# Kernel optimization log

Measured on AMD Instinct MI355X. Metric: run time of the kernel, lower is better.

The kernel has to match this reference:

```python
import jax, jax.numpy as jnp
import numpy as np
from jax import lax

K = 3
STRIDE = 1
PAD = 1


def setup_inputs() -> dict:
    key = jax.random.key(0)
    k0, k1, k2, k3 = jax.random.split(key, 4)
    B, C, H, W, O = 8, 128, 64, 64, 128
    x = jax.random.normal(k0, (B, C, H, W), jnp.float32)
    # offset_conv: Conv2d(C, 2*K*K) - small init so sampled offsets stay moderate
    w_off = jax.random.normal(k1, (2 * K * K, C, K, K), jnp.float32) * 0.01
    b_off = jnp.zeros((2 * K * K,), jnp.float32)
    # deform_conv main weight, kaiming-ish scale
    w_def = jax.random.normal(k2, (O, C, K, K), jnp.float32) * (1.0 / np.sqrt(C * K * K))
    b_def = jax.random.normal(k3, (O,), jnp.float32) * 0.01
    return {"x": x, "w_off": w_off, "b_off": b_off, "w_def": w_def, "b_def": b_def}


def _conv2d(x, w, b, stride, pad):
    y = lax.conv_general_dilated(
        x, w, window_strides=(stride, stride), padding=[(pad, pad), (pad, pad)],
        dimension_numbers=("NCHW", "OIHW", "NCHW"))
    return y + b[None, :, None, None]


def _bilinear_sample(x, py, px):
    """x: [B,C,Hin,Win]; py,px: [B,KK,H,W] -> [B,C,KK,H,W] with zero padding."""
    B, C, Hin, Win = x.shape
    iy0f = jnp.floor(py)
    ix0f = jnp.floor(px)
    wy = py - iy0f  # grad of floor is 0, so d(wy)/d(py) = 1 (matches deform conv)
    wx = px - ix0f
    iy0 = iy0f.astype(jnp.int32)
    ix0 = ix0f.astype(jnp.int32)

    def gather(iy, ix):
        valid = (iy >= 0) & (iy < Hin) & (ix >= 0) & (ix < Win)
        iyc = jnp.clip(iy, 0, Hin - 1)
        ixc = jnp.clip(ix, 0, Win - 1)
        g = jax.vmap(lambda xb, a, b: xb[:, a, b])(x, iyc, ixc)  # [B,C,KK,H,W]
        return g * valid[:, None].astype(x.dtype)

    v00 = gather(iy0, ix0)
    v01 = gather(iy0, ix0 + 1)
    v10 = gather(iy0 + 1, ix0)
    v11 = gather(iy0 + 1, ix0 + 1)
    wy_ = wy[:, None]
    wx_ = wx[:, None]
    return (v00 * (1 - wy_) * (1 - wx_) + v01 * (1 - wy_) * wx_
            + v10 * wy_ * (1 - wx_) + v11 * wy_ * wx_)


def reference(x, w_off, b_off, w_def, b_def):
    B, C, H, W = x.shape
    O = w_def.shape[0]
    KK = K * K
    # 1) standard conv predicting offsets: [B, 2*KK, Hout, Wout]
    offsets = _conv2d(x, w_off, b_off, STRIDE, PAD)
    Hout, Wout = offsets.shape[2], offsets.shape[3]
    # torchvision layout: interleaved (dy, dx) per kernel tap
    off = offsets.reshape(B, KK, 2, Hout, Wout)
    off_y, off_x = off[:, :, 0], off[:, :, 1]  # [B,KK,Hout,Wout]
    # 2) base sampling grid per kernel tap
    kys, kxs = jnp.meshgrid(jnp.arange(K), jnp.arange(K), indexing="ij")
    kys = kys.reshape(KK).astype(jnp.float32)
    kxs = kxs.reshape(KK).astype(jnp.float32)
    hs = (jnp.arange(Hout) * STRIDE - PAD).astype(jnp.float32)
    ws = (jnp.arange(Wout) * STRIDE - PAD).astype(jnp.float32)
    base_y = hs[None, :, None] + kys[:, None, None]  # [KK,Hout,1]
    base_x = ws[None, None, :] + kxs[:, None, None]  # [KK,1,Wout]
    py = base_y[None] + off_y  # [B,KK,Hout,Wout]
    px = base_x[None] + off_x
    # 3) gather bilinear-sampled patches then dense contraction (im2col GEMM)
    sampled = _bilinear_sample(x, py, px)  # [B,C,KK,Hout,Wout]
    out = jnp.einsum("bckhw,ock->bohw", sampled, w_def.reshape(O, C, KK))
    return out + b_def[None, :, None, None]
```

## Files before the change

### kernel.cpp

```cpp
#include <hip/hip_runtime.h>
#include <hip/hip_bf16.h>

#define BB 8
#define CC 128
#define HH 64
#define WW 64
#define OO 128
#define NJ 18
#define HW 4096

typedef unsigned short u16;
typedef unsigned int u32;
typedef __attribute__((ext_vector_type(8))) __bf16 bf16x8;
typedef __attribute__((ext_vector_type(4))) float f32x4;

__device__ __forceinline__ u16 f2bf(float f) {
    u32 u = __float_as_uint(f);
    u += 0x7fffu + ((u >> 16) & 1u);
    return (u16)(u >> 16);
}
__device__ __forceinline__ float bflo(u32 u) { return __uint_as_float(u << 16); }
__device__ __forceinline__ float bfhi(u32 u) { return __uint_as_float(u & 0xffff0000u); }
__device__ __forceinline__ u32 pk2bf(float s0, float s1) {
    union { __hip_bfloat162 h; u32 u; } cv;
    cv.h = __float22bfloat162_rn(make_float2(s0, s1));
    return cv.u;
}

__global__ __launch_bounds__(256)
void k_xT(const float* __restrict__ x, u16* __restrict__ xT) {
    __shared__ float tile[64][129];
    const int t = threadIdx.x;
    const int b = blockIdx.x >> 6;
    const int hw0 = (blockIdx.x & 63) << 6;
    const float* xb = x + (size_t)b * CC * HW + hw0;
    const int tw = t & 63, tc = t >> 6;
#pragma unroll
    for (int r = 0; r < 32; ++r) {
        int c = r * 4 + tc;
        tile[tw][c] = xb[c * HW + tw];
    }
    __syncthreads();
    u16* dst = xT + ((size_t)b * HW + hw0) * CC;
#pragma unroll
    for (int r = 0; r < 4; ++r) {
        int item = t + (r << 8);
        int seg = item & 15, hw = item >> 4;
        union { u32 d[4]; uint4 v; } p;
#pragma unroll
        for (int i = 0; i < 4; ++i)
            p.d[i] = pk2bf(tile[hw][seg * 8 + 2 * i], tile[hw][seg * 8 + 2 * i + 1]);
        *(uint4*)&dst[hw * CC + seg * 8] = p.v;
    }
}

__global__ void k_prep(const float* __restrict__ w_def,
                       const float* __restrict__ w_off,
                       u16* __restrict__ wT, u16* __restrict__ wA) {
    int idx = blockIdx.x * 256 + threadIdx.x;
    if (idx < 9 * OO * CC) {
        int c = idx & 127, o = (idx >> 7) & 127, kk = idx >> 14;
        wT[idx] = f2bf(w_def[(o * CC + c) * 9 + kk]);
    }
    if (idx < 32 * 1152) {
        int k = idx % 1152, j = idx / 1152;
        int q = k >> 7, c = k & 127;
        wA[idx] = (j < NJ) ? f2bf(w_off[(j * CC + c) * 9 + q]) : (u16)0;
    }
}

__global__ __launch_bounds__(256, 2)
void k_off(const u16* __restrict__ xT, const u16* __restrict__ wA,
           const float* __restrict__ b_off, float* __restrict__ offs) {
    __shared__ u16 s_x[198 * 128];
    const int t = threadIdx.x, lane = t & 63, wv = t >> 6;
    const int posl = lane & 15, kg = lane >> 4;
    const int b = blockIdx.x & 7, h = blockIdx.x >> 3;

    for (int it = t; it < 3168; it += 256) {
        int seg = it & 15, pix = it >> 4;
        int r = pix / 66, wp = pix - r * 66;
        int y = h - 1 + r, w = wp - 1;
        uint4 v = make_uint4(0, 0, 0, 0);
        if (y >= 0 && y < HH && w >= 0 && w < WW)
            v = *(const uint4*)&xT[((size_t)(b * HW) + y * WW + w) * CC + seg * 8];
        *(uint4*)&s_x[pix * 128 + ((seg ^ (pix & 15)) * 8)] = v;
    }
    __syncthreads();

    f32x4 acc0 = {0.f, 0.f, 0.f, 0.f}, acc1 = {0.f, 0.f, 0.f, 0.f};
    for (int q = 0; q < 9; ++q) {
        int qy = q / 3, qx = q - qy * 3;
        int pix = qy * 66 + (wv * 16 + posl) + qx;
        int prow = pix * 128, pxor = pix & 15;
#pragma unroll
        for (int ki = 0; ki < 4; ++ki) {
            int ks = q * 4 + ki;
            int cidx = ki * 4 + kg;
            bf16x8 bfr = *(const bf16x8*)&s_x[prow + ((cidx ^ pxor) * 8)];
            bf16x8 a0 = *(const bf16x8*)&wA[posl * 1152 + ks * 32 + kg * 8];
            bf16x8 a1 = *(const bf16x8*)&wA[(16 + posl) * 1152 + ks * 32 + kg * 8];
            acc0 = __builtin_amdgcn_mfma_f32_16x16x32_bf16(a0, bfr, acc0, 0, 0, 0);
            acc1 = __builtin_amdgcn_mfma_f32_16x16x32_bf16(a1, bfr, acc1, 0, 0, 0);
        }
    }
    const int pos = wv * 16 + posl;
#pragma unroll
    for (int r = 0; r < 4; ++r) {
        int j = kg * 4 + r;
        offs[(b * NJ + j) * HW + h * WW + pos] = acc0[r] + b_off[j];
    }
#pragma unroll
    for (int r = 0; r < 4; ++r) {
        int j = 16 + kg * 4 + r;
        if (j < NJ) offs[(b * NJ + j) * HW + h * WW + pos] = acc1[r] + b_off[j];
    }
}

__global__ __launch_bounds__(256, 3)
void k_main(const u16* __restrict__ xT, const float* __restrict__ offs,
            const u16* __restrict__ wT, const float* __restrict__ b_def,
            float* __restrict__ out) {
    __shared__ u16 s_wt[128 * 128];
    __shared__ u16 s_samp[16 * 520];

    const int t = threadIdx.x, lane = t & 63, wv = t >> 6;
    const int posl = lane & 15, rg = lane >> 4;
    const int b = blockIdx.x & 7;
    const int h = blockIdx.x >> 3;
    const int w = lane;
    const char* xb = (const char*)xT + (size_t)b * (HW * CC * 2);

    f32x4 acc[8];
#pragma unroll
    for (int mt = 0; mt < 8; ++mt) acc[mt] = (f32x4){0.f, 0.f, 0.f, 0.f};

    for (int kk = 0; kk < 9; ++kk) {
#pragma unroll
        for (int r = 0; r < 8; ++r) {
            int item = r * 256 + t;
            int o = item >> 4, sg = item & 15;
            *(uint4*)&s_wt[o * 128 + ((sg ^ (o & 15)) * 8)] =
                *(const uint4*)&wT[kk * (OO * CC) + item * 8];
        }
        int ky = kk / 3, kx = kk - ky * 3;
        float oy = offs[(b * NJ + 2 * kk) * HW + h * WW + w];
        float ox = offs[(b * NJ + 2 * kk + 1) * HW + h * WW + w];
        float py = (float)(h - 1 + ky) + oy;
        float px = (float)(w - 1 + kx) + ox;
        float fy = floorf(py), fx = floorf(px);
        int iy0 = (int)fy, ix0 = (int)fx;
        float wy = py - fy, wx = px - fx;
        int iy1 = iy0 + 1, ix1 = ix0 + 1;
        float my0 = (iy0 >= 0 && iy0 < HH) ? 1.0f : 0.0f;
        float my1 = (iy1 >= 0 && iy1 < HH) ? 1.0f : 0.0f;
        float mx0 = (ix0 >= 0 && ix0 < WW) ? 1.0f : 0.0f;
        float mx1 = (ix1 >= 0 && ix1 < WW) ? 1.0f : 0.0f;
        int iy0c = min(max(iy0, 0), HH - 1), iy1c = min(max(iy1, 0), HH - 1);
        int ix0c = min(max(ix0, 0), WW - 1), ix1c = min(max(ix1, 0), WW - 1);
        float wy1 = 1.0f - wy, wx1 = 1.0f - wx;
        float cwx = my0 * mx0 * wy1 * wx1, cwy = my0 * mx1 * wy1 * wx;
        float cwz = my1 * mx0 * wy * wx1,  cww = my1 * mx1 * wy * wx;
        int cox = (iy0c * WW + ix0c) << 8, coy = (iy0c * WW + ix1c) << 8;
        int coz = (iy1c * WW + ix0c) << 8, cow = (iy1c * WW + ix1c) << 8;

#pragma unroll
        for (int j = 0; j < 4; ++j) {
            const int seg = 4 * wv + j;
            const char* base = xb + seg * 16;
            uint4 q00 = *(const uint4*)(base + cox);
            uint4 q01 = *(const uint4*)(base + coy);
            uint4 q10 = *(const uint4*)(base + coz);
            uint4 q11 = *(const uint4*)(base + cow);
            const u32* u00 = (const u32*)&q00;
            const u32* u01 = (const u32*)&q01;
            const u32* u10 = (const u32*)&q10;
            const u32* u11 = (const u32*)&q11;
            union { u32 d[4]; uint4 v; } p;
#pragma unroll
            for (int i = 0; i < 4; ++i) {
                float s0 = cwx * bflo(u00[i]) + cwy * bflo(u01[i])
                         + cwz * bflo(u10[i]) + cww * bflo(u11[i]);
                float s1 = cwx * bfhi(u00[i]) + cwy * bfhi(u01[i])
                         + cwz * bfhi(u10[i]) + cww * bfhi(u11[i]);
                p.d[i] = pk2bf(s0, s1);
            }
            *(uint4*)&s_samp[seg * 520 + lane * 8] = p.v;
        }
        __syncthreads();

#pragma unroll
        for (int ct = 0; ct < 4; ++ct) {
            const int cidx = ct * 4 + rg;
            bf16x8 bfr = *(const bf16x8*)&s_samp[cidx * 520 + (wv * 16 + posl) * 8];
#pragma unroll
            for (int mt = 0; mt < 8; ++mt) {
                bf16x8 af = *(const bf16x8*)&s_wt[(mt * 16 + posl) * 128 + ((cidx ^ posl) * 8)];
                acc[mt] = __builtin_amdgcn_mfma_f32_16x16x32_bf16(af, bfr, acc[mt], 0, 0, 0);
            }
        }
        __syncthreads();
    }

    const int wout = wv * 16 + posl;
#pragma unroll
    for (int mt = 0; mt < 8; ++mt) {
#pragma unroll
        for (int r = 0; r < 4; ++r) {
            int o = mt * 16 + rg * 4 + r;
            out[((b * OO + o) * HH + h) * WW + wout] = acc[mt][r] + b_def[o];
        }
    }
}

extern "C" void kernel_launch(void* const* d_in, const int* in_sizes, int n_in,
                              void* d_out, int out_size, void* d_ws, size_t ws_size,
                              hipStream_t stream) {
    const float* x     = (const float*)d_in[0];
    const float* w_off = (const float*)d_in[1];
    const float* b_off = (const float*)d_in[2];
    const float* w_def = (const float*)d_in[3];
    const float* b_def = (const float*)d_in[4];
    float* out = (float*)d_out;

    float* offs = (float*)d_ws;
    u16*   xT   = (u16*)(offs + BB * NJ * HW);
    u16*   wT   = xT + (size_t)BB * HW * CC;
    u16*   wA   = wT + 9 * OO * CC;

    k_xT  <<<512, 256, 0, stream>>>(x, xT);
    k_prep<<<576, 256, 0, stream>>>(w_def, w_off, wT, wA);
    k_off <<<512, 256, 0, stream>>>(xT, wA, b_off, offs);
    k_main<<<512, 256, 0, stream>>>(xT, offs, wT, b_def, out);
}
```

Measured before the change: 159.7 us.

## Load weight fragments directly to registers and swap MFMA operand roles in main kernel

Removes the per-tap staging of the 128x128 weight slice into shared memory; each wave now reads its 32-output-channel slice of weights straight from global memory into registers. Sampled patches become the A operand (positions along M) with an XOR-swizzled 64x128 layout, and the sampling work is redistributed so four threads share a position and each handles four channel segments. Outputs are written as float4 along width. This shrinks LDS use and the sync-heavy weight copy, at the cost of global (L2) weight reads per wave and a lower launch-bounds occupancy hint.

```diff
diff --git a/kernel.cpp b/kernel.cpp
--- a/kernel.cpp
+++ b/kernel.cpp
@@ -117,37 +117,35 @@
     }
 }
 
-__global__ __launch_bounds__(256, 3)
+__global__ __launch_bounds__(256, 2)
 void k_main(const u16* __restrict__ xT, const float* __restrict__ offs,
             const u16* __restrict__ wT, const float* __restrict__ b_def,
             float* __restrict__ out) {
-    __shared__ u16 s_wt[128 * 128];
-    __shared__ u16 s_samp[16 * 520];
+    __shared__ u16 s_samp[64 * 128];
 
     const int t = threadIdx.x, lane = t & 63, wv = t >> 6;
-    const int posl = lane & 15, rg = lane >> 4;
+    const int posl = lane & 15, kg = lane >> 4;
     const int b = blockIdx.x & 7;
     const int h = blockIdx.x >> 3;
-    const int w = lane;
     const char* xb = (const char*)xT + (size_t)b * (HW * CC * 2);
 
-    f32x4 acc[8];
-#pragma unroll
-    for (int mt = 0; mt < 8; ++mt) acc[mt] = (f32x4){0.f, 0.f, 0.f, 0.f};
-
+    const int gpos = t >> 2;
+    const int segsub = t & 3;
+
+    f32x4 acc[4][2];
+#pragma unroll
+    for (int mt = 0; mt < 4; ++mt) {
+        acc[mt][0] = (f32x4){0.f, 0.f, 0.f, 0.f};
+        acc[mt][1] = (f32x4){0.f, 0.f, 0.f, 0.f};
+    }
+
+#pragma unroll 1
     for (int kk = 0; kk < 9; ++kk) {
-#pragma unroll
-        for (int r = 0; r < 8; ++r) {
-            int item = r * 256 + t;
-            int o = item >> 4, sg = item & 15;
-            *(uint4*)&s_wt[o * 128 + ((sg ^ (o & 15)) * 8)] =
-                *(const uint4*)&wT[kk * (OO * CC) + item * 8];
-        }
         int ky = kk / 3, kx = kk - ky * 3;
-        float oy = offs[(b * NJ + 2 * kk) * HW + h * WW + w];
-        float ox = offs[(b * NJ + 2 * kk + 1) * HW + h * WW + w];
+        float oy = offs[(b * NJ + 2 * kk) * HW + h * WW + gpos];
+        float ox = offs[(b * NJ + 2 * kk + 1) * HW + h * WW + gpos];
         float py = (float)(h - 1 + ky) + oy;
-        float px = (float)(w - 1 + kx) + ox;
+        float px = (float)(gpos - 1 + kx) + ox;
         float fy = floorf(py), fx = floorf(px);
         int iy0 = (int)fy, ix0 = (int)fx;
         float wy = py - fy, wx = px - fx;
@@ -164,14 +162,16 @@
         int cox = (iy0c * WW + ix0c) << 8, coy = (iy0c * WW + ix1c) << 8;
         int coz = (iy1c * WW + ix0c) << 8, cow = (iy1c * WW + ix1c) << 8;
 
+        const int slotbase = gpos * 128;
+        const int pxor = gpos & 15;
 #pragma unroll
         for (int j = 0; j < 4; ++j) {
-            const int seg = 4 * wv + j;
-            const char* base = xb + seg * 16;
-            uint4 q00 = *(const uint4*)(base + cox);
-            uint4 q01 = *(const uint4*)(base + coy);
-            uint4 q10 = *(const uint4*)(base + coz);
-            uint4 q11 = *(const uint4*)(base + cow);
+            const int seg = segsub + 4 * j;
+            const int sb = seg * 16;
+            uint4 q00 = *(const uint4*)(xb + cox + sb);
+            uint4 q01 = *(const uint4*)(xb + coy + sb);
+            uint4 q10 = *(const uint4*)(xb + coz + sb);
+            uint4 q11 = *(const uint4*)(xb + cow + sb);
             const u32* u00 = (const u32*)&q00;
             const u32* u01 = (const u32*)&q01;
             const u32* u10 = (const u32*)&q10;
@@ -185,30 +185,52 @@
                          + cwz * bfhi(u10[i]) + cww * bfhi(u11[i]);
                 p.d[i] = pk2bf(s0, s1);
             }
-            *(uint4*)&s_samp[seg * 520 + lane * 8] = p.v;
+            *(uint4*)&s_samp[slotbase + ((seg ^ pxor) * 8)] = p.v;
         }
         __syncthreads();
 
-#pragma unroll
-        for (int ct = 0; ct < 4; ++ct) {
-            const int cidx = ct * 4 + rg;
-            bf16x8 bfr = *(const bf16x8*)&s_samp[cidx * 520 + (wv * 16 + posl) * 8];
-#pragma unroll
-            for (int mt = 0; mt < 8; ++mt) {
-                bf16x8 af = *(const bf16x8*)&s_wt[(mt * 16 + posl) * 128 + ((cidx ^ posl) * 8)];
-                acc[mt] = __builtin_amdgcn_mfma_f32_16x16x32_bf16(af, bfr, acc[mt], 0, 0, 0);
+        {
+            const int o0 = wv * 32;
+            const u16* wkk = wT + kk * (OO * CC);
+            bf16x8 wfr[4][2];
+#pragma unroll
+            for (int ct = 0; ct < 4; ++ct) {
+#pragma unroll
+                for (int nt = 0; nt < 2; ++nt) {
+                    int o = o0 + nt * 16 + posl;
+                    wfr[ct][nt] = *(const bf16x8*)&wkk[o * CC + ct * 32 + kg * 8];
+                }
             }
+#pragma unroll
+            for (int ct = 0; ct < 4; ++ct) {
+                const int chunk = ct * 4 + kg;
+#pragma unroll
+                for (int mt = 0; mt < 4; ++mt) {
+                    bf16x8 afr = *(const bf16x8*)
+                        &s_samp[(mt * 16 + posl) * 128 + ((chunk ^ posl) * 8)];
+                    acc[mt][0] = __builtin_amdgcn_mfma_f32_16x16x32_bf16(
+                        afr, wfr[ct][0], acc[mt][0], 0, 0, 0);
+                    acc[mt][1] = __builtin_amdgcn_mfma_f32_16x16x32_bf16(
+                        afr, wfr[ct][1], acc[mt][1], 0, 0, 0);
+                }
+            }
         }
         __syncthreads();
     }
 
-    const int wout = wv * 16 + posl;
-#pragma unroll
-    for (int mt = 0; mt < 8; ++mt) {
-#pragma unroll
-        for (int r = 0; r < 4; ++r) {
-            int o = mt * 16 + rg * 4 + r;
-            out[((b * OO + o) * HH + h) * WW + wout] = acc[mt][r] + b_def[o];
+#pragma unroll
+    for (int nt = 0; nt < 2; ++nt) {
+        const int o = wv * 32 + nt * 16 + posl;
+        const float bd = b_def[o];
+        float* orow = out + ((b * OO + o) * HH + h) * WW;
+#pragma unroll
+        for (int mt = 0; mt < 4; ++mt) {
+            float4 res;
+            res.x = acc[mt][nt][0] + bd;
+            res.y = acc[mt][nt][1] + bd;
+            res.z = acc[mt][nt][2] + bd;
+            res.w = acc[mt][nt][3] + bd;
+            *(float4*)&orow[mt * 16 + kg * 4] = res;
         }
     }
 }
```

After: 139.5 us. -12.6%, faster.
